# Kernel optimization log

Hardware: AMD Instinct MI355X
Metric: run time of the kernel (lower is better)

## Reference

```python
import jax, jax.numpy as jnp
import numpy as np

HEADS = 16
DIM_HEAD = 64
SCALE = DIM_HEAD ** -0.5
STEP = 0.6

def setup_inputs() -> dict:
    key = jax.random.key(0)
    ks = jax.random.split(key, 8)
    B, N, QD = 2, 2048, 1024
    M, CD = 1024, 768
    inner = HEADS * DIM_HEAD  # 1024
    return {
        "x": jax.random.normal(ks[0], (B, N, QD), jnp.float32),
        "context": jax.random.normal(ks[1], (B, M, CD), jnp.float32),
        "focused_attention_mask": jax.random.uniform(ks[2], (1, M, M), jnp.float32),
        "Wq": jax.random.normal(ks[3], (inner, QD), jnp.float32) * 0.02,
        "Wk": jax.random.normal(ks[4], (inner, CD), jnp.float32) * 0.02,
        "Wv": jax.random.normal(ks[5], (inner, CD), jnp.float32) * 0.02,
        "Wo": jax.random.normal(ks[6], (QD, inner), jnp.float32) * 0.02,
        "bo": jax.random.normal(ks[7], (QD,), jnp.float32) * 0.02,
    }

def _split_heads(t, h):
    b, n, hd = t.shape
    return t.reshape(b, n, h, hd // h).transpose(0, 2, 1, 3).reshape(b * h, n, hd // h)

def reference(x, context, focused_attention_mask, Wq, Wk, Wv, Wo, bo):
    b, n, _ = x.shape
    h = HEADS
    q = _split_heads(x @ Wq.T, h)        # (b h) n d
    k = _split_heads(context @ Wk.T, h)  # (b h) m d
    v = _split_heads(context @ Wv.T, h)
    sim = jnp.einsum('bid,bjd->bij', q, k) * SCALE  # (b h) n m
    # FCA focus-weight modulation (fam has leading dim 1, broadcast over b*h)
    fam = focused_attention_mask[0]  # (m, m)
    K = fam.shape[-1]
    fw = jnp.abs(jnp.einsum('bqk,dk->bqd', sim[:, :, :K], fam))  # (b h) n m
    fw = jnp.minimum(fw, 1.0)
    fw = fw / (jnp.max(fw, axis=2, keepdims=True) + 1e-6)
    fw = (fw > STEP).astype(sim.dtype)
    sim = sim.at[:, :, :K].add((fw - 1.0) * 50.0)
    attn = jax.nn.softmax(sim, axis=-1)
    out = jnp.einsum('bij,bjd->bid', attn, v)  # (b h) n d
    out = out.reshape(b, h, n, -1).transpose(0, 2, 1, 3).reshape(b, n, -1)
    return out @ Wo.T + bo
```

## Files before the change

### kernel.cpp

```cpp
#include <hip/hip_runtime.h>
#include <hip/hip_fp16.h>
#include <math.h>

#define SCALE 0.125f

typedef _Float16 f16;
typedef __attribute__((ext_vector_type(8))) _Float16 f16x8;
typedef __attribute__((ext_vector_type(4))) float f32x4;

#define MFMA(a, b, c) __builtin_amdgcn_mfma_f32_16x16x32_f16((a), (b), (c), 0, 0, 0)

__device__ __forceinline__ void gll16(const f16* g, f16* l) {
    __builtin_amdgcn_global_load_lds(
        (const __attribute__((address_space(1))) unsigned int*)(g),
        (__attribute__((address_space(3))) unsigned int*)(l),
        16, 0, 0);
}

struct SplitSeg { const float* src; f16* h; f16* l; float scale; size_t n; };
struct SplitArgs { SplitSeg seg[7]; };

__global__ __launch_bounds__(256) void split_all(SplitArgs a)
{
    SplitSeg s = a.seg[blockIdx.y];
    size_t i4 = ((size_t)blockIdx.x * 256 + threadIdx.x) * 4;
    size_t stride = (size_t)gridDim.x * 256 * 4;
    for (; i4 < s.n; i4 += stride) {
        float4 v = *(const float4*)&s.src[i4];
        float av[4] = {v.x * s.scale, v.y * s.scale, v.z * s.scale, v.w * s.scale};
        f16 hv[4], lv[4];
#pragma unroll
        for (int j = 0; j < 4; ++j) {
            hv[j] = (f16)av[j];
            lv[j] = (f16)(av[j] - (float)hv[j]);
        }
        *(float2*)&s.h[i4] = *(float2*)hv;
        *(float2*)&s.l[i4] = *(float2*)lv;
    }
}

#define GX(r, g) (((r) << 5) + ((((g) ^ ((r) & 3))) << 3))

template <int AP, int BP>
__global__ __launch_bounds__(256) void gemm16(
    const f16* __restrict__ Ah, const f16* __restrict__ Al, size_t Abat,
    const f16* __restrict__ Bh, const f16* __restrict__ Bl, int Bstr, size_t Bbat,
    float* __restrict__ Cf, const float* __restrict__ bias,
    f16* __restrict__ Ch, f16* __restrict__ Cl, int Cpitch,
    f16* __restrict__ Cth, f16* __restrict__ Ctl, int Mt,
    int Nsplit, f16* __restrict__ C2th, int Mt2,
    size_t Cbat, float oscale, int M, int N, int K)
{
    constexpr int NCH = AP * 8 + BP * 4;
    __shared__ __align__(16) f16 Ash[AP][128 * 32];
    __shared__ __align__(16) f16 Bsh[BP][64 * 32];

    const int tid  = threadIdx.x;
    const int z    = blockIdx.z;
    Ah += z * Abat; if (AP == 2) Al += z * Abat;
    Bh += z * Bbat; if (BP == 2) Bl += z * Bbat;
    const int m0   = blockIdx.y * 128;
    const int n0   = blockIdx.x * 64;
    const int w    = tid >> 6;
    const int lane = tid & 63;
    const int wm   = (w >> 1) * 64;
    const int wn   = (w & 1) * 32;
    const int lq   = lane >> 4;
    const int l15  = lane & 15;

    f32x4 acc[4][2];
#pragma unroll
    for (int mi = 0; mi < 4; ++mi)
#pragma unroll
        for (int ni = 0; ni < 2; ++ni) acc[mi][ni] = (f32x4){0.f, 0.f, 0.f, 0.f};

    for (int k0 = 0; k0 < K; k0 += 32) {
        __syncthreads();
#pragma unroll
        for (int c = 0; c < NCH / 4; ++c) {
            int chunk = c * 4 + w;
            const f16* gp; f16* lp;
            if (chunk < AP * 8) {
                int pl = chunk >> 3, sub = chunk & 7;
                int r = sub * 16 + (lane >> 2);
                int g = (lane & 3) ^ (r & 3);
                gp = ((AP == 2 && pl) ? Al : Ah) + (size_t)(m0 + r) * K + k0 + g * 8;
                lp = &Ash[pl][sub * 512];
            } else {
                int cb = chunk - AP * 8;
                int pl = cb >> 2, sub = cb & 3;
                int r = sub * 16 + (lane >> 2);
                int g = (lane & 3) ^ (r & 3);
                gp = ((BP == 2 && pl) ? Bl : Bh) + (size_t)(n0 + r) * Bstr + k0 + g * 8;
                lp = &Bsh[pl][sub * 512];
            }
            gll16(gp, lp);
        }
        __syncthreads();

        f16x8 afh[4], afl[4];
#pragma unroll
        for (int mi = 0; mi < 4; ++mi) {
            int r = wm + mi * 16 + l15;
            afh[mi] = *(const f16x8*)&Ash[0][GX(r, lq)];
            if (AP == 2) afl[mi] = *(const f16x8*)&Ash[1][GX(r, lq)];
        }
#pragma unroll
        for (int ni = 0; ni < 2; ++ni) {
            int r = wn + ni * 16 + l15;
            f16x8 bh = *(const f16x8*)&Bsh[0][GX(r, lq)];
            f16x8 bl;
            if (BP == 2) bl = *(const f16x8*)&Bsh[1][GX(r, lq)];
#pragma unroll
            for (int mi = 0; mi < 4; ++mi) {
                f32x4 a = acc[mi][ni];
                a = MFMA(afh[mi], bh, a);
                if (BP == 2) a = MFMA(afh[mi], bl, a);
                if (AP == 2) a = MFMA(afl[mi], bh, a);
                acc[mi][ni] = a;
            }
        }
    }

    const bool vhalf = (Nsplit > 0) && (n0 >= Nsplit);
    if (Cf)  Cf  += z * Cbat;
    if (Ch)  { Ch += z * Cbat; if (Cl) Cl += z * Cbat; }

#pragma unroll
    for (int mi = 0; mi < 4; ++mi) {
#pragma unroll
        for (int ni = 0; ni < 2; ++ni) {
            int row = m0 + wm + mi * 16 + lq * 4;
            int col = n0 + wn + ni * 16 + l15;
            float v[4];
#pragma unroll
            for (int r = 0; r < 4; ++r) v[r] = acc[mi][ni][r] * oscale;
            if (Cf) {
                float bb = bias ? bias[col] : 0.f;
#pragma unroll
                for (int r = 0; r < 4; ++r)
                    Cf[(size_t)(row + r) * Cpitch + col] = v[r] + bb;
            } else if (vhalf) {
                union { f16 a[4]; float2 f; } uh;
#pragma unroll
                for (int r = 0; r < 4; ++r) uh.a[r] = (f16)v[r];
                *(float2*)&C2th[(size_t)(col - Nsplit) * Mt2 + row] = uh.f;
            } else {
                if (Ch) {
#pragma unroll
                    for (int r = 0; r < 4; ++r) {
                        f16 hh = (f16)v[r];
                        Ch[(size_t)(row + r) * Cpitch + col] = hh;
                        if (Cl) Cl[(size_t)(row + r) * Cpitch + col] = (f16)(v[r] - (float)hh);
                    }
                }
                if (Cth) {
                    union { f16 a[4]; float2 f; } uh, ul;
#pragma unroll
                    for (int r = 0; r < 4; ++r) {
                        uh.a[r] = (f16)v[r];
                        ul.a[r] = (f16)(v[r] - (float)uh.a[r]);
                    }
                    *(float2*)&Cth[(size_t)col * Mt + row] = uh.f;
                    if (Ctl) *(float2*)&Ctl[(size_t)col * Mt + row] = ul.f;
                }
            }
        }
    }
}

#define LX(r, qd) (((r) << 6) + ((((qd) ^ ((r) & 7))) << 3))

__global__ __launch_bounds__(256) void attn_mfma(
    const f16* __restrict__ Qh, const f16* __restrict__ Ql,
    const f16* __restrict__ Kh,
    const f16* __restrict__ Gh, const f16* __restrict__ Gl,
    const f16* __restrict__ Vth, f16* __restrict__ AOh)
{
    __shared__ __align__(16) f16 Ksh[4096];
    __shared__ __align__(16) f16 Gsh[2][4096];
    __shared__ __align__(16) f16 Ps[128 * 72];

    const int tid = threadIdx.x;
    const int bh = blockIdx.x;
    const int b = bh >> 4, h = bh & 15;
    const int qr0 = blockIdx.y * 128;
    const int w = tid >> 6, lane = tid & 63;
    const int lq = lane >> 4, l15 = lane & 15;
    const int wq = w * 32;

    const size_t qb = ((size_t)(b * 2048 + qr0)) * 1024 + h * 64;
    const size_t kb = ((size_t)(b * 1024)) * 1024 + h * 64;
    const size_t vb = (size_t)(h * 64) * 2048 + b * 1024;

    const int sr = lane >> 3;
    const int ss = lane & 7;

    f16x8 aqh[2][2], aql[2][2];
#pragma unroll
    for (int ti = 0; ti < 2; ++ti)
#pragma unroll
        for (int kc = 0; kc < 2; ++kc) {
            size_t off = qb + (size_t)(wq + ti * 16 + l15) * 1024 + (kc * 4 + lq) * 8;
            aqh[ti][kc] = *(const f16x8*)&Qh[off];
            aql[ti][kc] = *(const f16x8*)&Ql[off];
        }

    float mx[2][4] = {};
    for (int jt = 0; jt < 16; ++jt) {
        __syncthreads();
#pragma unroll
        for (int c = 0; c < 4; ++c) {
            int chunk = c * 4 + w;
            int pl = chunk >> 3, sub = chunk & 7;
            int r = sub * 8 + sr;
            int g = ss ^ (r & 7);
            const f16* gp = (pl ? Gl : Gh) + kb + (size_t)(jt * 64 + r) * 1024 + g * 8;
            gll16(gp, &Gsh[pl][sub * 512]);
        }
        __syncthreads();

#pragma unroll
        for (int tj = 0; tj < 4; ++tj) {
            f32x4 a0 = {0.f, 0.f, 0.f, 0.f}, a1 = {0.f, 0.f, 0.f, 0.f};
#pragma unroll
            for (int kc = 0; kc < 2; ++kc) {
                int lx = LX(tj * 16 + l15, kc * 4 + lq);
                f16x8 bgh = *(const f16x8*)&Gsh[0][lx];
                f16x8 bgl = *(const f16x8*)&Gsh[1][lx];
                a0 = MFMA(aqh[0][kc], bgh, a0);
                a0 = MFMA(aqh[0][kc], bgl, a0);
                a0 = MFMA(aql[0][kc], bgh, a0);
                a1 = MFMA(aqh[1][kc], bgh, a1);
                a1 = MFMA(aqh[1][kc], bgl, a1);
                a1 = MFMA(aql[1][kc], bgh, a1);
            }
#pragma unroll
            for (int r = 0; r < 4; ++r) {
                mx[0][r] = fmaxf(mx[0][r], fminf(fabsf(a0[r] * SCALE), 1.f));
                mx[1][r] = fmaxf(mx[1][r], fminf(fabsf(a1[r] * SCALE), 1.f));
            }
        }
    }
    float inv[2][4];
#pragma unroll
    for (int ti = 0; ti < 2; ++ti)
#pragma unroll
        for (int r = 0; r < 4; ++r) {
            float m = mx[ti][r];
#pragma unroll
            for (int d = 1; d < 16; d <<= 1)
                m = fmaxf(m, __shfl_xor(m, d, 64));
            inv[ti][r] = 1.0f / (m + 1e-6f);
        }

    f32x4 aco[2][4];
#pragma unroll
    for (int ti = 0; ti < 2; ++ti)
#pragma unroll
        for (int dj = 0; dj < 4; ++dj) aco[ti][dj] = (f32x4){0.f, 0.f, 0.f, 0.f};
    float dsum[2][4] = {};

    for (int jt = 0; jt < 16; ++jt) {
        __syncthreads();
#pragma unroll
        for (int c = 0; c < 6; ++c) {
            int chunk = c * 4 + w;
            int sub = chunk & 7;
            int r = sub * 8 + sr;
            int g = ss ^ (r & 7);
            size_t off = kb + (size_t)(jt * 64 + r) * 1024 + g * 8;
            const f16* gp; f16* lp;
            if (chunk < 8)       { gp = Kh + off; lp = &Ksh[sub * 512]; }
            else if (chunk < 16) { gp = Gh + off; lp = &Gsh[0][sub * 512]; }
            else                 { gp = Gl + off; lp = &Gsh[1][sub * 512]; }
            gll16(gp, lp);
        }
        __syncthreads();

#pragma unroll
        for (int tj = 0; tj < 4; ++tj) {
            f32x4 s0 = {0.f, 0.f, 0.f, 0.f}, s1 = {0.f, 0.f, 0.f, 0.f};
            f32x4 f0 = {0.f, 0.f, 0.f, 0.f}, f1 = {0.f, 0.f, 0.f, 0.f};
#pragma unroll
            for (int kc = 0; kc < 2; ++kc) {
                int lx = LX(tj * 16 + l15, kc * 4 + lq);
                f16x8 bkh = *(const f16x8*)&Ksh[lx];
                f16x8 bgh = *(const f16x8*)&Gsh[0][lx];
                f16x8 bgl = *(const f16x8*)&Gsh[1][lx];
                s0 = MFMA(aqh[0][kc], bkh, s0);
                f0 = MFMA(aqh[0][kc], bgh, f0);
                f0 = MFMA(aqh[0][kc], bgl, f0);
                f0 = MFMA(aql[0][kc], bgh, f0);
                s1 = MFMA(aqh[1][kc], bkh, s1);
                f1 = MFMA(aqh[1][kc], bgh, f1);
                f1 = MFMA(aqh[1][kc], bgl, f1);
                f1 = MFMA(aql[1][kc], bgh, f1);
            }
#pragma unroll
            for (int r = 0; r < 4; ++r) {
                float fn0 = fminf(fabsf(f0[r] * SCALE), 1.f) * inv[0][r];
                f16 e0 = (f16)__expf(s0[r] * SCALE + (fn0 > 0.6f ? 0.f : -50.f));
                Ps[(wq + lq * 4 + r) * 72 + tj * 16 + l15] = e0;
                dsum[0][r] += (float)e0;
                float fn1 = fminf(fabsf(f1[r] * SCALE), 1.f) * inv[1][r];
                f16 e1 = (f16)__expf(s1[r] * SCALE + (fn1 > 0.6f ? 0.f : -50.f));
                Ps[(wq + 16 + lq * 4 + r) * 72 + tj * 16 + l15] = e1;
                dsum[1][r] += (float)e1;
            }
        }
        __syncthreads();
#pragma unroll
        for (int c = 0; c < 2; ++c) {
            int chunk = c * 4 + w;
            int sub = chunk & 7;
            int r = sub * 8 + sr;
            int g = ss ^ (r & 7);
            const f16* gp = Vth + vb + (size_t)r * 2048 + jt * 64 + g * 8;
            gll16(gp, &Ksh[sub * 512]);
        }
        __syncthreads();

#pragma unroll
        for (int kc = 0; kc < 2; ++kc) {
            f16x8 ap0 = *(const f16x8*)&Ps[(wq + l15) * 72 + kc * 32 + lq * 8];
            f16x8 ap1 = *(const f16x8*)&Ps[(wq + 16 + l15) * 72 + kc * 32 + lq * 8];
#pragma unroll
            for (int dj = 0; dj < 4; ++dj) {
                int lx = LX(dj * 16 + l15, kc * 4 + lq);
                f16x8 bvh = *(const f16x8*)&Ksh[lx];
                aco[0][dj] = MFMA(ap0, bvh, aco[0][dj]);
                aco[1][dj] = MFMA(ap1, bvh, aco[1][dj]);
            }
        }
    }

#pragma unroll
    for (int ti = 0; ti < 2; ++ti)
#pragma unroll
        for (int r = 0; r < 4; ++r) {
            float s = dsum[ti][r];
#pragma unroll
            for (int d = 1; d < 16; d <<= 1)
                s += __shfl_xor(s, d, 64);
            dsum[ti][r] = s;
        }
#pragma unroll
    for (int ti = 0; ti < 2; ++ti) {
#pragma unroll
        for (int r = 0; r < 4; ++r) {
            float invd = 1.0f / dsum[ti][r];
            int qq = qr0 + wq + ti * 16 + lq * 4 + r;
#pragma unroll
            for (int dj = 0; dj < 4; ++dj) {
                int dd = h * 64 + dj * 16 + l15;
                AOh[(size_t)(b * 2048 + qq) * 1024 + dd] = (f16)(aco[ti][dj][r] * invd);
            }
        }
    }
}

extern "C" void kernel_launch(void* const* d_in, const int* in_sizes, int n_in,
                              void* d_out, int out_size, void* d_ws, size_t ws_size,
                              hipStream_t stream)
{
    const float* x   = (const float*)d_in[0];
    const float* ctx = (const float*)d_in[1];
    const float* fam = (const float*)d_in[2];
    const float* Wq  = (const float*)d_in[3];
    const float* Wk  = (const float*)d_in[4];
    const float* Wv  = (const float*)d_in[5];
    const float* Wo  = (const float*)d_in[6];
    const float* bo  = (const float*)d_in[7];
    float* out = (float*)d_out;

    const size_t nX  = (size_t)4096 * 1024;
    const size_t nC  = (size_t)2048 * 768;
    const size_t nWq = (size_t)1024 * 1024;
    const size_t nWk = (size_t)1024 * 768;
    const size_t nF  = (size_t)1024 * 1024;
    const size_t nK  = (size_t)2048 * 1024;

    char* p = (char*)d_ws;
    f16 *xh   = (f16*)p; p += nX * 2;   f16 *xl   = (f16*)p; p += nX * 2;
    f16 *ch   = (f16*)p; p += nC * 2;   f16 *cl   = (f16*)p; p += nC * 2;
    f16 *wqh  = (f16*)p; p += nWq * 2;  f16 *wql  = (f16*)p; p += nWq * 2;
    f16 *wkvh = (f16*)p; p += nWk * 4;  f16 *wkvl = (f16*)p; p += nWk * 4;
    f16 *woh  = (f16*)p; p += nWq * 2;  f16 *wol  = (f16*)p; p += nWq * 2;
    f16 *fmh  = (f16*)p; p += nF * 2;   f16 *fml  = (f16*)p; p += nF * 2;
    f16 *qh   = (f16*)p; p += nX * 2;   f16 *ql   = (f16*)p; p += nX * 2;
    f16 *kh   = (f16*)p; p += nK * 2;
    f16 *kth  = (f16*)p; p += nK * 2;   f16 *ktl  = (f16*)p; p += nK * 2;
    f16 *vth  = (f16*)p; p += nK * 2;
    f16 *gh   = (f16*)p; p += nK * 2;   f16 *gl   = (f16*)p; p += nK * 2;
    f16 *aoh  = (f16*)p; p += nX * 2;

    const float WS  = 64.0f;
    const float IWS = 1.0f / 64.0f;

    SplitArgs sa;
    sa.seg[0] = {x,   xh,          xl,          1.f, nX};
    sa.seg[1] = {ctx, ch,          cl,          1.f, nC};
    sa.seg[2] = {Wq,  wqh,         wql,         WS,  nWq};
    sa.seg[3] = {Wk,  wkvh,        wkvl,        WS,  nWk};
    sa.seg[4] = {Wv,  wkvh + nWk,  wkvl + nWk,  WS,  nWk};
    sa.seg[5] = {Wo,  woh,         wol,         WS,  nWq};
    sa.seg[6] = {fam, fmh,         fml,         1.f, nF};
    split_all<<<dim3(64, 7), 256, 0, stream>>>(sa);

    gemm16<2, 2><<<dim3(16, 32, 1), 256, 0, stream>>>(
        xh, xl, 0, wqh, wql, 1024, 0,
        nullptr, nullptr, qh, ql, 1024, nullptr, nullptr, 0,
        0, nullptr, 0, 0, IWS, 4096, 1024, 1024);

    gemm16<2, 2><<<dim3(32, 16, 1), 256, 0, stream>>>(
        ch, cl, 0, wkvh, wkvl, 768, 0,
        nullptr, nullptr, kh, nullptr, 1024, kth, ktl, 2048,
        1024, vth, 2048, 0, IWS, 2048, 2048, 768);

    gemm16<2, 2><<<dim3(16, 8, 2), 256, 0, stream>>>(
        fmh, fml, 0, kth, ktl, 2048, 1024,
        nullptr, nullptr, gh, gl, 1024, nullptr, nullptr, 0,
        0, nullptr, 0, (size_t)1024 * 1024, 1.f, 1024, 1024, 1024);

    attn_mfma<<<dim3(32, 16), 256, 0, stream>>>(qh, ql, kh, gh, gl, vth, aoh);

    gemm16<1, 1><<<dim3(16, 32, 1), 256, 0, stream>>>(
        aoh, nullptr, 0, woh, nullptr, 1024, 0,
        out, bo, nullptr, nullptr, 1024, nullptr, nullptr, 0,
        0, nullptr, 0, 0, IWS, 4096, 1024, 1024);
}
```

Baseline: 320.5 us.

## Deepen GEMM K-tile, early-exit focus-max pass, simplify mask threshold test

The projection GEMM now stages 64-wide K slices with an 8-way XOR swizzle, halving the number of barrier-separated load rounds. In attention, the first pass that finds the per-row focus-weight max now reduces each tile and stops once every row in the block has reached the clamp value of 1, since the max cannot grow past it. The mask test is rewritten as a comparison of |f| against a precomputed threshold, and the exponent uses exp2 with folded constants. The early exit only helps when clamped values appear early, and the per-tile shuffle reductions and barrier add overhead when they do not.

```diff
diff --git a/kernel.cpp b/kernel.cpp
--- a/kernel.cpp
+++ b/kernel.cpp
@@ -9,6 +9,8 @@
 typedef __attribute__((ext_vector_type(4))) float f32x4;
 
 #define MFMA(a, b, c) __builtin_amdgcn_mfma_f32_16x16x32_f16((a), (b), (c), 0, 0, 0)
+
+#define LX(r, qd) (((r) << 6) + ((((qd) ^ ((r) & 7))) << 3))
 
 __device__ __forceinline__ void gll16(const f16* g, f16* l) {
     __builtin_amdgcn_global_load_lds(
@@ -38,8 +40,6 @@
         *(float2*)&s.l[i4] = *(float2*)lv;
     }
 }
-
-#define GX(r, g) (((r) << 5) + ((((g) ^ ((r) & 3))) << 3))
 
 template <int AP, int BP>
 __global__ __launch_bounds__(256) void gemm16(
@@ -51,9 +51,9 @@
     int Nsplit, f16* __restrict__ C2th, int Mt2,
     size_t Cbat, float oscale, int M, int N, int K)
 {
-    constexpr int NCH = AP * 8 + BP * 4;
-    __shared__ __align__(16) f16 Ash[AP][128 * 32];
-    __shared__ __align__(16) f16 Bsh[BP][64 * 32];
+    constexpr int NCH = AP * 16 + BP * 8;
+    __shared__ __align__(16) f16 Ash[AP][128 * 64];
+    __shared__ __align__(16) f16 Bsh[BP][64 * 64];
 
     const int tid  = threadIdx.x;
     const int z    = blockIdx.z;
@@ -67,6 +67,8 @@
     const int wn   = (w & 1) * 32;
     const int lq   = lane >> 4;
     const int l15  = lane & 15;
+    const int sr   = lane >> 3;
+    const int sg   = lane & 7;
 
     f32x4 acc[4][2];
 #pragma unroll
@@ -74,23 +76,23 @@
 #pragma unroll
         for (int ni = 0; ni < 2; ++ni) acc[mi][ni] = (f32x4){0.f, 0.f, 0.f, 0.f};
 
-    for (int k0 = 0; k0 < K; k0 += 32) {
+    for (int k0 = 0; k0 < K; k0 += 64) {
         __syncthreads();
 #pragma unroll
         for (int c = 0; c < NCH / 4; ++c) {
             int chunk = c * 4 + w;
             const f16* gp; f16* lp;
-            if (chunk < AP * 8) {
-                int pl = chunk >> 3, sub = chunk & 7;
-                int r = sub * 16 + (lane >> 2);
-                int g = (lane & 3) ^ (r & 3);
+            if (chunk < AP * 16) {
+                int pl = chunk >> 4, sub = chunk & 15;
+                int r = sub * 8 + sr;
+                int g = sg ^ (r & 7);
                 gp = ((AP == 2 && pl) ? Al : Ah) + (size_t)(m0 + r) * K + k0 + g * 8;
                 lp = &Ash[pl][sub * 512];
             } else {
-                int cb = chunk - AP * 8;
-                int pl = cb >> 2, sub = cb & 3;
-                int r = sub * 16 + (lane >> 2);
-                int g = (lane & 3) ^ (r & 3);
+                int cb = chunk - AP * 16;
+                int pl = cb >> 3, sub = cb & 7;
+                int r = sub * 8 + sr;
+                int g = sg ^ (r & 7);
                 gp = ((BP == 2 && pl) ? Bl : Bh) + (size_t)(n0 + r) * Bstr + k0 + g * 8;
                 lp = &Bsh[pl][sub * 512];
             }
@@ -98,26 +100,29 @@
         }
         __syncthreads();
 
-        f16x8 afh[4], afl[4];
-#pragma unroll
-        for (int mi = 0; mi < 4; ++mi) {
-            int r = wm + mi * 16 + l15;
-            afh[mi] = *(const f16x8*)&Ash[0][GX(r, lq)];
-            if (AP == 2) afl[mi] = *(const f16x8*)&Ash[1][GX(r, lq)];
-        }
-#pragma unroll
-        for (int ni = 0; ni < 2; ++ni) {
-            int r = wn + ni * 16 + l15;
-            f16x8 bh = *(const f16x8*)&Bsh[0][GX(r, lq)];
-            f16x8 bl;
-            if (BP == 2) bl = *(const f16x8*)&Bsh[1][GX(r, lq)];
+#pragma unroll
+        for (int kc = 0; kc < 2; ++kc) {
+            f16x8 afh[4], afl[4];
 #pragma unroll
             for (int mi = 0; mi < 4; ++mi) {
-                f32x4 a = acc[mi][ni];
-                a = MFMA(afh[mi], bh, a);
-                if (BP == 2) a = MFMA(afh[mi], bl, a);
-                if (AP == 2) a = MFMA(afl[mi], bh, a);
-                acc[mi][ni] = a;
+                int r = wm + mi * 16 + l15;
+                afh[mi] = *(const f16x8*)&Ash[0][LX(r, kc * 4 + lq)];
+                if (AP == 2) afl[mi] = *(const f16x8*)&Ash[1][LX(r, kc * 4 + lq)];
+            }
+#pragma unroll
+            for (int ni = 0; ni < 2; ++ni) {
+                int r = wn + ni * 16 + l15;
+                f16x8 bh = *(const f16x8*)&Bsh[0][LX(r, kc * 4 + lq)];
+                f16x8 bl;
+                if (BP == 2) bl = *(const f16x8*)&Bsh[1][LX(r, kc * 4 + lq)];
+#pragma unroll
+                for (int mi = 0; mi < 4; ++mi) {
+                    f32x4 a = acc[mi][ni];
+                    a = MFMA(afh[mi], bh, a);
+                    if (BP == 2) a = MFMA(afh[mi], bl, a);
+                    if (AP == 2) a = MFMA(afl[mi], bh, a);
+                    acc[mi][ni] = a;
+                }
             }
         }
     }
@@ -168,8 +173,6 @@
         }
     }
 }
-
-#define LX(r, qd) (((r) << 6) + ((((qd) ^ ((r) & 7))) << 3))
 
 __global__ __launch_bounds__(256) void attn_mfma(
     const f16* __restrict__ Qh, const f16* __restrict__ Ql,
@@ -180,6 +183,7 @@
     __shared__ __align__(16) f16 Ksh[4096];
     __shared__ __align__(16) f16 Gsh[2][4096];
     __shared__ __align__(16) f16 Ps[128 * 72];
+    __shared__ int eflag[4];
 
     const int tid = threadIdx.x;
     const int bh = blockIdx.x;
@@ -208,7 +212,6 @@
 
     float mx[2][4] = {};
     for (int jt = 0; jt < 16; ++jt) {
-        __syncthreads();
 #pragma unroll
         for (int c = 0; c < 4; ++c) {
             int chunk = c * 4 + w;
@@ -241,19 +244,32 @@
                 mx[1][r] = fmaxf(mx[1][r], fminf(fabsf(a1[r] * SCALE), 1.f));
             }
         }
-    }
-    float inv[2][4];
+        bool done = true;
+#pragma unroll
+        for (int ti = 0; ti < 2; ++ti)
+#pragma unroll
+            for (int r = 0; r < 4; ++r) {
+                float m = mx[ti][r];
+#pragma unroll
+                for (int d = 1; d < 16; d <<= 1)
+                    m = fmaxf(m, __shfl_xor(m, d, 64));
+                mx[ti][r] = m;
+                done = done && (m >= 1.0f);
+            }
+        int wd = __all(done ? 1 : 0);
+        if (lane == 0) eflag[w] = wd;
+        __syncthreads();
+        if (eflag[0] && eflag[1] && eflag[2] && eflag[3]) break;
+    }
+    float T[2][4];
 #pragma unroll
     for (int ti = 0; ti < 2; ++ti)
 #pragma unroll
-        for (int r = 0; r < 4; ++r) {
-            float m = mx[ti][r];
-#pragma unroll
-            for (int d = 1; d < 16; d <<= 1)
-                m = fmaxf(m, __shfl_xor(m, d, 64));
-            inv[ti][r] = 1.0f / (m + 1e-6f);
-        }
-
+        for (int r = 0; r < 4; ++r)
+            T[ti][r] = 4.8f * (mx[ti][r] + 1e-6f);
+
+    const float SL2E = 0.125f * 1.44269504088896f;
+    const float PEN2 = -50.0f * 1.44269504088896f;
     f32x4 aco[2][4];
 #pragma unroll
     for (int ti = 0; ti < 2; ++ti)
@@ -299,12 +315,12 @@
             }
 #pragma unroll
             for (int r = 0; r < 4; ++r) {
-                float fn0 = fminf(fabsf(f0[r] * SCALE), 1.f) * inv[0][r];
-                f16 e0 = (f16)__expf(s0[r] * SCALE + (fn0 > 0.6f ? 0.f : -50.f));
+                float p0 = (fabsf(f0[r]) > T[0][r]) ? 0.f : PEN2;
+                f16 e0 = (f16)exp2f(fmaf(s0[r], SL2E, p0));
                 Ps[(wq + lq * 4 + r) * 72 + tj * 16 + l15] = e0;
                 dsum[0][r] += (float)e0;
-                float fn1 = fminf(fabsf(f1[r] * SCALE), 1.f) * inv[1][r];
-                f16 e1 = (f16)__expf(s1[r] * SCALE + (fn1 > 0.6f ? 0.f : -50.f));
+                float p1 = (fabsf(f1[r]) > T[1][r]) ? 0.f : PEN2;
+                f16 e1 = (f16)exp2f(fmaf(s1[r], SL2E, p1));
                 Ps[(wq + 16 + lq * 4 + r) * 72 + tj * 16 + l15] = e1;
                 dsum[1][r] += (float)e1;
             }
```

New measurement: 286.3 us. -10.7%, faster.
